# Kernel optimization log

Hardware: AMD Instinct MI355X
Metric: run time of the kernel (lower is better)

## Reference

```python
import jax, jax.numpy as jnp
import numpy as np

D_MODEL = 192
NODE_NUM = 64
DEPTH = 2
ALPHA = 0.05
NUM_LAYERS = 2
LN_EPS = 1e-5


def _gcn(x, p):
    # x: [N, in_dim*D_MODEL]; faithful port of GCN.forward (eval mode)
    nv1, nv2, ws, bs, wm, bm, we, be, wl, bl, g, b = p
    N = x.shape[0]
    in_dim = x.shape[1] // D_MODEL
    adp = jax.nn.softmax(jax.nn.relu(nv1 @ nv2), axis=1)            # [V,V]
    adj = adp + jnp.eye(NODE_NUM, dtype=x.dtype)
    a = adj / adj.sum(1, keepdims=True)                              # row-normalized
    h0 = jax.lax.conv_general_dilated(
        x.reshape(N, in_dim, D_MODEL), ws, (1,), 'VALID',
        dimension_numbers=('NCH', 'OIH', 'NCH')) + bs[None, :, None]  # [N,C,V]
    h = h0
    outs = [h0]
    for _ in range(DEPTH):
        h = ALPHA * h0 + (1.0 - ALPHA) * jnp.einsum('ncw,vw->ncv', h, a)
        outs.append(h)
    ho = jnp.concatenate(outs, axis=1)                               # [N,(DEPTH+1)C,V]
    ho = jax.nn.gelu(jnp.einsum('ncv,oc->nov', ho, wm) + bm[None, :, None], approximate=False)
    ho = jnp.einsum('ncv,oc->nov', ho, we) + be[None, :, None]       # [N,6,V]
    ho = jnp.einsum('nov,dv->nod', ho, wl) + bl                      # [N,6,D]
    mu = ho.mean(-1, keepdims=True)
    var = ((ho - mu) ** 2).mean(-1, keepdims=True)                   # biased, like torch LN
    ho = (ho - mu) / jnp.sqrt(var + LN_EPS) * g + b
    return ho.reshape(N, 6 * D_MODEL)


def _encoder(inp4, flag, layer_params):
    x = jnp.transpose(inp4, (2, 0, 1, 3)) if flag == 1 else jnp.transpose(inp4, (1, 0, 2, 3))
    W, B, O, D = x.shape
    L = W + O - 1
    N = W * B
    # input_transfer: shift row r by r along the slice axis
    place = jax.vmap(lambda xr, r: jax.lax.dynamic_update_slice(
        jnp.zeros((B, L, D), x.dtype), xr, (0, r, 0)))
    a = place(x, jnp.arange(W)).reshape(N, L, D)
    layer0_output = None
    output_all = None
    rows_layers, cols_layers = [], []
    for layer in range(NUM_LAYERS):
        if layer >= 1:
            a = output_all  # eval mode: F.dropout is identity
            if layer == 1:
                layer0_output = a
        p = layer_params[layer]

        def step(carry, x_t, p=p):
            h_row, h_col = carry
            gate = _gcn(jnp.concatenate([h_row, h_col, x_t], axis=-1), p)  # [N,6D]
            sg = jax.nn.sigmoid(gate[:, :4 * D])
            tg = jnp.tanh(gate[:, 4 * D:])
            ug_r, og_r, ug_c, og_c = jnp.split(sg, 4, axis=-1)
            ig_r, ig_c = jnp.split(tg, 2, axis=-1)
            h_row = jnp.tanh((1.0 - ug_r) * h_row + ug_r * ig_r) * og_r
            h_col = jnp.tanh((1.0 - ug_c) * h_col + ug_c * ig_c) * og_c
            out_s = jnp.concatenate([h_row, h_col], axis=-1)
            # col hidden is saved pre-roll, rolled for next step
            return (h_row, jnp.roll(h_col, B, axis=0)), (out_s, h_row, h_col)

        init = (jnp.zeros((N, D), x.dtype), jnp.zeros((N, D), x.dtype))
        _, (outs, hrows, hcols) = jax.lax.scan(step, init, jnp.swapaxes(a, 0, 1))
        output_all = jnp.swapaxes(outs, 0, 1)                        # [N,L,2D]
        if layer >= 1:
            output_all = output_all + layer0_output
        # rows saved at slice s>=O-1 from block loc = s-O+1
        rows = hrows.reshape(L, W, B, D)[jnp.arange(O - 1, L), jnp.arange(W)]  # [W,B,D]
        # cols saved at slice s>=W-1 from last batch block
        cols = hcols[W - 1:, (W - 1) * B:, :]                        # [O,B,D]
        rows_layers.append(rows)
        cols_layers.append(cols)
    hidden_row_all = jnp.stack(rows_layers).transpose(2, 0, 1, 3)    # [B,layers,W,D]
    hidden_col_all = jnp.stack(cols_layers).transpose(2, 0, 1, 3)    # [B,layers,O,D]
    if flag == 1:
        return output_all, hidden_col_all, hidden_row_all
    return output_all, hidden_row_all, hidden_col_all


def setup_inputs() -> dict:
    key = jax.random.key(0)
    ks = jax.random.split(key, 20)
    idx = [0]
    def nxt():
        k = ks[idx[0]]
        idx[0] += 1
        return k
    B, W, O = 8, 24, 48
    K = D_MODEL - NODE_NUM + 1  # 129
    cc, sc, nd = 16, 32, 40
    d = {"input": jax.random.normal(nxt(), (B, W, O, D_MODEL), dtype=jnp.float32)}
    for li, in_dim in enumerate([3, 4]):
        d[f"nodevec1_{li}"] = jax.random.normal(nxt(), (NODE_NUM, nd), dtype=jnp.float32)
        d[f"nodevec2_{li}"] = jax.random.normal(nxt(), (nd, NODE_NUM), dtype=jnp.float32)
        d[f"w_start_{li}"] = jax.random.normal(nxt(), (cc, in_dim, K), dtype=jnp.float32) * 0.05
        d[f"b_start_{li}"] = jnp.zeros((cc,), jnp.float32)
        d[f"w_mlp_{li}"] = jax.random.normal(nxt(), (sc, (DEPTH + 1) * cc), dtype=jnp.float32) * 0.05
        d[f"b_mlp_{li}"] = jnp.zeros((sc,), jnp.float32)
        d[f"w_end_{li}"] = jax.random.normal(nxt(), (6, sc), dtype=jnp.float32) * 0.05
        d[f"b_end_{li}"] = jnp.zeros((6,), jnp.float32)
        d[f"w_lin_{li}"] = jax.random.normal(nxt(), (D_MODEL, NODE_NUM), dtype=jnp.float32) * 0.05
        d[f"b_lin_{li}"] = jnp.zeros((D_MODEL,), jnp.float32)
        d[f"gamma_{li}"] = jnp.ones((D_MODEL,), jnp.float32)
        d[f"beta_{li}"] = jnp.zeros((D_MODEL,), jnp.float32)
    d["flag"] = 0
    return d


def reference(input, nodevec1_0, nodevec2_0, w_start_0, b_start_0, w_mlp_0, b_mlp_0,
              w_end_0, b_end_0, w_lin_0, b_lin_0, gamma_0, beta_0,
              nodevec1_1, nodevec2_1, w_start_1, b_start_1, w_mlp_1, b_mlp_1,
              w_end_1, b_end_1, w_lin_1, b_lin_1, gamma_1, beta_1, flag):
    p0 = (nodevec1_0, nodevec2_0, w_start_0, b_start_0, w_mlp_0, b_mlp_0,
          w_end_0, b_end_0, w_lin_0, b_lin_0, gamma_0, beta_0)
    p1 = (nodevec1_1, nodevec2_1, w_start_1, b_start_1, w_mlp_1, b_mlp_1,
          w_end_1, b_end_1, w_lin_1, b_lin_1, gamma_1, beta_1)
    return _encoder(input, flag, (p0, p1))
```

## Files before the change

kernel.cpp:

```cpp
#include <hip/hip_runtime.h>
#include <hip/hip_bf16.h>

#define NT 512
typedef unsigned short u16;

__device__ __forceinline__ u16 tobf(float x) {
  union { __hip_bfloat16 h; u16 u; } cv;
  cv.h = __float2bfloat16(x);
  return cv.u;
}
__device__ __forceinline__ float frombf(u16 u) {
  return __uint_as_float(((unsigned)u) << 16);
}
__device__ __forceinline__ float sigf(float x) {
  return __builtin_amdgcn_rcpf(1.f + __builtin_amdgcn_exp2f(-1.4426950408889634f * x));
}
__device__ __forceinline__ float tanh_fast(float x) {
  return 1.f - 2.f * __builtin_amdgcn_rcpf(1.f + __builtin_amdgcn_exp2f(2.8853900817779268f * x));
}

struct SeqArgs {
  const float* input;
  const float* nv1_0; const float* nv2_0; const float* nv1_1; const float* nv2_1;
  const float* w_start0; const float* b_start0; const float* w_mlp0; const float* b_mlp0;
  const float* w_end0;   const float* b_end0;   const float* w_lin0; const float* b_lin0;
  const float* gamma0;   const float* beta0;
  const float* w_start1; const float* b_start1; const float* w_mlp1; const float* b_mlp1;
  const float* w_end1;   const float* b_end1;   const float* w_lin1; const float* b_lin1;
  const float* gamma1;   const float* beta1;
  float* HCOL;
  int*   flags;
  float* out_all; float* out_hrow; float* out_hcol;
};

__global__ __launch_bounds__(NT, 2) void seq_kernel(SeqArgs A) {
  const int n = blockIdx.x, w = n >> 3, b = n & 7, tid = threadIdx.x;
  const int pred = (n + 184) % 192;

  __shared__ __align__(16) float sCIN[768];
  __shared__ __align__(16) u16   sWS[64 * 132];
  __shared__ __align__(16) float sAT[4096];
  __shared__ __align__(16) float sH[2][1024];
  __shared__ __align__(16) float sAbuf[4928];
  float* const sPart = sAbuf;
  float* const sG    = sAbuf;
  float* const sE    = sAbuf + 2048;
  float* const sY    = sAbuf;
  float* const smWE  = sAbuf + 3072;
  float* const smBE  = sAbuf + 3264;
  float* const smWM  = sAbuf + 3328;

  for (int layer = 0; layer < 2; ++layer) {
    const int in_dim = 3 + layer;
    const int P = in_dim - 1;
    const float* nv1    = layer ? A.nv1_1    : A.nv1_0;
    const float* nv2    = layer ? A.nv2_1    : A.nv2_0;
    const float* wstart = layer ? A.w_start1 : A.w_start0;
    const float* bs     = layer ? A.b_start1 : A.b_start0;
    const float* wm     = layer ? A.w_mlp1   : A.w_mlp0;
    const float* bm     = layer ? A.b_mlp1   : A.b_mlp0;
    const float* we     = layer ? A.w_end1   : A.w_end0;
    const float* be     = layer ? A.b_end1   : A.b_end0;
    const float* wl     = layer ? A.w_lin1   : A.w_lin0;
    const float* bl     = layer ? A.b_lin1   : A.b_lin0;
    const float* gm     = layer ? A.gamma1   : A.gamma0;
    const float* bt     = layer ? A.beta1    : A.beta0;

    for (int idx = tid; idx < 4096; idx += NT) {
      int v = idx >> 6, ww = idx & 63;
      float s = 0.f;
      for (int j = 0; j < 40; ++j) s = fmaf(nv1[v*40 + j], nv2[j*64 + ww], s);
      sAbuf[idx] = fmaxf(s, 0.f);
    }
    __syncthreads();
    if (tid < 64) {
      const int v = tid;
      float m = -1e30f;
      for (int ww = 0; ww < 64; ++ww) m = fmaxf(m, sAbuf[v*64 + ww]);
      float s = 0.f;
      for (int ww = 0; ww < 64; ++ww) { float e = expf(sAbuf[v*64 + ww] - m); sAbuf[v*64 + ww] = e; s += e; }
      float inv = 1.f / s, rs = 1.f;
      for (int ww = 0; ww < 64; ++ww) rs += sAbuf[v*64 + ww] * inv;
      float irs = 1.f / rs;
      for (int ww = 0; ww < 64; ++ww) {
        float a = sAbuf[v*64 + ww] * inv + ((ww == v) ? 1.f : 0.f);
        sAT[ww*64 + v] = a * irs;
      }
    }
    __syncthreads();
    for (int idx = tid; idx < 16*in_dim*132; idx += NT) {
      int row = idx / 132, k = idx - row*132;
      sWS[idx] = (k < 129) ? tobf(wstart[((row & 15)*in_dim + (row >> 4))*129 + k]) : (u16)0;
    }
    for (int idx = tid; idx < 1536; idx += NT) { int o = idx/48, c = idx - o*48; smWM[o*50 + c] = wm[idx]; }
    for (int idx = tid; idx < 192; idx += NT) smWE[idx] = we[idx];
    if (tid < 6) smBE[tid] = be[tid];
    for (int d = tid; d < 384; d += NT) sCIN[d] = 0.f;

    const int v_p = tid & 63;
    const int o0  = tid >> 6;
    const float bmv0 = bm[o0], bmv1 = bm[o0 + 8], bmv2 = bm[o0 + 16], bmv3 = bm[o0 + 24];
    float blv = 0.f, gmv = 1.f, btv = 0.f;
    if (tid < 384) blv = bl[(tid >= 192) ? tid - 192 : tid];
    if (tid < 192) { gmv = gm[tid]; btv = bt[tid]; }
    float bs_r[2];
    bs_r[0] = bs[tid >> 6];
    bs_r[1] = bs[(tid >> 6) + 8];
    __syncthreads();

    auto pre_phase = [&](int t) {
      if (layer == 0) {
        int o = t - w;
        if (o >= 0 && o < 48) {
          const float* xr = A.input + (((size_t)(b*24 + w)*48 + o)*192);
          for (int d = tid; d < 192; d += NT) sCIN[384 + d] = xr[d];
        } else {
          for (int d = tid; d < 192; d += NT) sCIN[384 + d] = 0.f;
        }
      } else {
        const float* xr = A.out_all + ((size_t)n*71 + t)*384;
        for (int d = tid; d < 384; d += NT) sCIN[384 + d] = xr[d];
      }
      __syncthreads();
      const int nslots = P << 8;
      for (int s = tid; s < nslots; s += NT) {
        const int cidx = s >> 4;
        const int p = cidx >> 4, c = cidx & 15;
        const int vg = s & 15;
        const int ich = (p == 0) ? 0 : (p + 1);
        const float* xin = ((p == 0) ? &sCIN[0] : &sCIN[384 + (p-1)*192]) + vg*4;
        const u16* wrow = &sWS[(ich*16 + c)*132];
        float a0 = 0.f, a1 = 0.f, a2 = 0.f, a3 = 0.f;
        float4 xc = *(const float4*)xin;
        for (int k4 = 0; k4 < 128; k4 += 4) {
          ushort4 wu = *(const ushort4*)(wrow + k4);
          float w0 = frombf(wu.x), w1 = frombf(wu.y), w2 = frombf(wu.z), w3 = frombf(wu.w);
          float4 xn = *(const float4*)(xin + k4 + 4);
          a0 = fmaf(w3, xc.w, fmaf(w2, xc.z, fmaf(w1, xc.y, fmaf(w0, xc.x, a0))));
          a1 = fmaf(w3, xn.x, fmaf(w2, xc.w, fmaf(w1, xc.z, fmaf(w0, xc.y, a1))));
          a2 = fmaf(w3, xn.y, fmaf(w2, xn.x, fmaf(w1, xc.w, fmaf(w0, xc.z, a2))));
          a3 = fmaf(w3, xn.z, fmaf(w2, xn.y, fmaf(w1, xn.x, fmaf(w0, xc.w, a3))));
          xc = xn;
        }
        float wk = frombf(wrow[128]);
        a0 = fmaf(wk, xc.x, a0); a1 = fmaf(wk, xc.y, a1);
        a2 = fmaf(wk, xc.z, a2); a3 = fmaf(wk, xc.w, a3);
        *(float4*)&sPart[cidx*64 + vg*4] = make_float4(a0, a1, a2, a3);
      }
      __syncthreads();
      {
        const int c0 = tid >> 6, v = tid & 63;
        float sum0 = bs_r[0], sum1 = bs_r[1];
        for (int p = 0; p < P; ++p) {
          sum0 += sPart[(p*16 + c0     )*64 + v];
          sum1 += sPart[(p*16 + c0 + 8 )*64 + v];
        }
        sH[0][ c0      *64 + v] = sum0;
        sH[0][(c0 + 8 )*64 + v] = sum1;
      }
      __syncthreads();
    };
    pre_phase(0);

    for (int t = 0; t < 71; ++t) {
      const int S = layer*71 + t;

      if (t > 0) {
        if (tid == 0) {
          while (__hip_atomic_load(&A.flags[pred*32], __ATOMIC_ACQUIRE, __HIP_MEMORY_SCOPE_AGENT) < S)
            __builtin_amdgcn_s_sleep(1);
        }
        __syncthreads();
        float* hc = A.HCOL + ((size_t)((S-1) & 31)*192 + pred)*192;
        for (int d = tid; d < 192; d += NT)
          sCIN[192 + d] = __hip_atomic_load(&hc[d], __ATOMIC_RELAXED, __HIP_MEMORY_SCOPE_AGENT);
        __syncthreads();
      }

      {
        const int c = tid >> 5, vg2 = tid & 31;
        const int vbase = c*64 + vg2*2;
        const float* xin = &sCIN[192 + vg2*2];
        const u16* wrow = &sWS[(16 + c)*132];
        float a0 = sH[0][vbase], a1 = sH[0][vbase + 1];
        float2 xc = *(const float2*)xin;
        for (int k2 = 0; k2 < 128; k2 += 2) {
          ushort2 wu = *(const ushort2*)(wrow + k2);
          float w0 = frombf(wu.x), w1 = frombf(wu.y);
          float2 xn = *(const float2*)(xin + k2 + 2);
          a0 = fmaf(w1, xc.y, fmaf(w0, xc.x, a0));
          a1 = fmaf(w1, xn.x, fmaf(w0, xc.y, a1));
          xc = xn;
        }
        float wk = frombf(wrow[128]);
        a0 = fmaf(wk, xc.x, a0); a1 = fmaf(wk, xc.y, a1);
        sH[0][vbase] = a0; sH[0][vbase + 1] = a1;
      }
      __syncthreads();

      float g0 = bmv0, g1 = bmv1, g2 = bmv2, g3 = bmv3;
      {
        const int c0 = o0 * 2;
        float pa0 = 0.f, pa1 = 0.f;
        for (int w4 = 0; w4 < 64; w4 += 4) {
          float a0v = sAT[(w4+0)*64 + v_p];
          float a1v = sAT[(w4+1)*64 + v_p];
          float a2v = sAT[(w4+2)*64 + v_p];
          float a3v = sAT[(w4+3)*64 + v_p];
          float4 h0v = *(const float4*)&sH[0][ c0      *64 + w4];
          float4 h1v = *(const float4*)&sH[0][(c0 + 1 )*64 + w4];
          pa0 = fmaf(h0v.x, a0v, pa0); pa0 = fmaf(h0v.y, a1v, pa0);
          pa0 = fmaf(h0v.z, a2v, pa0); pa0 = fmaf(h0v.w, a3v, pa0);
          pa1 = fmaf(h1v.x, a0v, pa1); pa1 = fmaf(h1v.y, a1v, pa1);
          pa1 = fmaf(h1v.z, a2v, pa1); pa1 = fmaf(h1v.w, a3v, pa1);
        }
        sH[1][ c0      *64 + v_p] = fmaf(0.95f, pa0, 0.05f * sH[0][ c0      *64 + v_p]);
        sH[1][(c0 + 1 )*64 + v_p] = fmaf(0.95f, pa1, 0.05f * sH[0][(c0 + 1 )*64 + v_p]);
        for (int c = 0; c < 16; ++c) {
          float hv = sH[0][c*64 + v_p];
          g0 = fmaf(smWM[(o0     )*50 + c], hv, g0);
          g1 = fmaf(smWM[(o0 +  8)*50 + c], hv, g1);
          g2 = fmaf(smWM[(o0 + 16)*50 + c], hv, g2);
          g3 = fmaf(smWM[(o0 + 24)*50 + c], hv, g3);
        }
      }
      __syncthreads();

      {
        const int c0 = o0 * 2;
        float pa0 = 0.f, pa1 = 0.f;
        for (int w4 = 0; w4 < 64; w4 += 4) {
          float a0v = sAT[(w4+0)*64 + v_p];
          float a1v = sAT[(w4+1)*64 + v_p];
          float a2v = sAT[(w4+2)*64 + v_p];
          float a3v = sAT[(w4+3)*64 + v_p];
          float4 h0v = *(const float4*)&sH[1][ c0      *64 + w4];
          float4 h1v = *(const float4*)&sH[1][(c0 + 1 )*64 + w4];
          pa0 = fmaf(h0v.x, a0v, pa0); pa0 = fmaf(h0v.y, a1v, pa0);
          pa0 = fmaf(h0v.z, a2v, pa0); pa0 = fmaf(h0v.w, a3v, pa0);
          pa1 = fmaf(h1v.x, a0v, pa1); pa1 = fmaf(h1v.y, a1v, pa1);
          pa1 = fmaf(h1v.z, a2v, pa1); pa1 = fmaf(h1v.w, a3v, pa1);
        }
        float h00 = sH[0][ c0      *64 + v_p];
        float h01 = sH[0][(c0 + 1 )*64 + v_p];
        sH[0][ c0      *64 + v_p] = fmaf(0.95f, pa0, 0.05f * h00);
        sH[0][(c0 + 1 )*64 + v_p] = fmaf(0.95f, pa1, 0.05f * h01);
        for (int c = 0; c < 16; ++c) {
          float hv = sH[1][c*64 + v_p];
          g0 = fmaf(smWM[(o0     )*50 + 16 + c], hv, g0);
          g1 = fmaf(smWM[(o0 +  8)*50 + 16 + c], hv, g1);
          g2 = fmaf(smWM[(o0 + 16)*50 + 16 + c], hv, g2);
          g3 = fmaf(smWM[(o0 + 24)*50 + 16 + c], hv, g3);
        }
      }
      __syncthreads();

      {
        for (int c = 0; c < 16; ++c) {
          float hv = sH[0][c*64 + v_p];
          g0 = fmaf(smWM[(o0     )*50 + 32 + c], hv, g0);
          g1 = fmaf(smWM[(o0 +  8)*50 + 32 + c], hv, g1);
          g2 = fmaf(smWM[(o0 + 16)*50 + 32 + c], hv, g2);
          g3 = fmaf(smWM[(o0 + 24)*50 + 32 + c], hv, g3);
        }
        g0 = 0.5f * g0 * (1.f + erff(g0 * 0.70710678118654752f));
        g1 = 0.5f * g1 * (1.f + erff(g1 * 0.70710678118654752f));
        g2 = 0.5f * g2 * (1.f + erff(g2 * 0.70710678118654752f));
        g3 = 0.5f * g3 * (1.f + erff(g3 * 0.70710678118654752f));
        sG[(o0     )*64 + v_p] = g0;
        sG[(o0 +  8)*64 + v_p] = g1;
        sG[(o0 + 16)*64 + v_p] = g2;
        sG[(o0 + 24)*64 + v_p] = g3;
      }
      __syncthreads();

      for (int idx = tid; idx < 384; idx += NT) {
        int o2 = idx >> 6, v = idx & 63;
        float acc = smBE[o2];
        for (int c = 0; c < 32; ++c) acc = fmaf(smWE[o2*32 + c], sG[c*64 + v], acc);
        sE[idx] = acc;
      }
      __syncthreads();

      if (tid < 384) {
        const int d  = (tid >= 192) ? tid - 192 : tid;
        const int r0 = (tid >= 192) ? 3 : 0;
        const float4* wrow = (const float4*)(wl + d*64);
        float y0 = blv, y1 = blv, y2 = blv;
        for (int q = 0; q < 16; ++q) {
          float4 wv = wrow[q];
          float4 e0 = *(const float4*)&sE[(r0+0)*64 + q*4];
          float4 e1 = *(const float4*)&sE[(r0+1)*64 + q*4];
          float4 e2 = *(const float4*)&sE[(r0+2)*64 + q*4];
          y0 = fmaf(e0.x,wv.x, fmaf(e0.y,wv.y, fmaf(e0.z,wv.z, fmaf(e0.w,wv.w, y0))));
          y1 = fmaf(e1.x,wv.x, fmaf(e1.y,wv.y, fmaf(e1.z,wv.z, fmaf(e1.w,wv.w, y1))));
          y2 = fmaf(e2.x,wv.x, fmaf(e2.y,wv.y, fmaf(e2.z,wv.z, fmaf(e2.w,wv.w, y2))));
        }
        sY[(r0+0)*192 + d] = y0;
        sY[(r0+1)*192 + d] = y1;
        sY[(r0+2)*192 + d] = y2;
      }
      __syncthreads();

      if (tid < 192) {
        const int r = tid >> 5, l32 = tid & 31;
        float sm = 0.f, sq = 0.f;
#pragma unroll
        for (int m = 0; m < 6; ++m) {
          float v = sY[r*192 + l32 + 32*m];
          sm += v; sq = fmaf(v, v, sq);
        }
#pragma unroll
        for (int off = 16; off >= 1; off >>= 1) {
          sm += __shfl_xor(sm, off);
          sq += __shfl_xor(sq, off);
        }
        if (l32 == 0) {
          float mu = sm * (1.f/192.f);
          float var = sq * (1.f/192.f) - mu*mu;
          sH[1][r] = mu;
          sH[1][8 + r] = rsqrtf(fmaxf(var, 0.f) + 1e-5f);
        }
      }
      __syncthreads();

      float hcn = 0.f;
      if (tid < 192) {
        const int d = tid;
        float y2 = fmaf((sY[2*192+d] - sH[1][2]) * sH[1][10], gmv, btv);
        float y3 = fmaf((sY[3*192+d] - sH[1][3]) * sH[1][11], gmv, btv);
        float y5 = fmaf((sY[5*192+d] - sH[1][5]) * sH[1][13], gmv, btv);
        float ugc = sigf(y2), ogc = sigf(y3), igc = tanh_fast(y5);
        float hc = sCIN[192 + d];
        hcn = tanh_fast(fmaf(ugc, igc, (1.f - ugc)*hc)) * ogc;
        __hip_atomic_store(&A.HCOL[((size_t)(S & 31)*192 + n)*192 + d], hcn,
                           __ATOMIC_RELAXED, __HIP_MEMORY_SCOPE_AGENT);
      }
      __syncthreads();
      if (tid == 0) {
        __threadfence();
        __hip_atomic_store(&A.flags[n*32], S + 1, __ATOMIC_RELEASE, __HIP_MEMORY_SCOPE_AGENT);
      }
      if (tid < 192) {
        const int d = tid;
        float y0 = fmaf((sY[0*192+d] - sH[1][0]) * sH[1][8],  gmv, btv);
        float y1 = fmaf((sY[1*192+d] - sH[1][1]) * sH[1][9],  gmv, btv);
        float y4 = fmaf((sY[4*192+d] - sH[1][4]) * sH[1][12], gmv, btv);
        float ugr = sigf(y0), ogr = sigf(y1), igr = tanh_fast(y4);
        float hr = sCIN[d];
        float hrn = tanh_fast(fmaf(ugr, igr, (1.f - ugr)*hr)) * ogr;
        sCIN[d] = hrn;
        float* oa = A.out_all + ((size_t)n*71 + t)*384;
        if (layer == 0) { oa[d] = hrn; oa[192 + d] = hcn; }
        else           { oa[d] = hrn + sCIN[384 + d]; oa[192 + d] = hcn + sCIN[576 + d]; }
        if (t == 47 + w)
          A.out_hrow[(((size_t)b*2 + layer)*24 + w)*192 + d] = hrn;
        if (w == 23 && t >= 23)
          A.out_hcol[(((size_t)b*2 + layer)*48 + (t - 23))*192 + d] = hcn;
      }
      __syncthreads();
      if (t < 70) pre_phase(t + 1);
    }
    __syncthreads();
  }
}

extern "C" void kernel_launch(void* const* d_in, const int* in_sizes, int n_in,
                              void* d_out, int out_size, void* d_ws, size_t ws_size,
                              hipStream_t stream) {
  (void)in_sizes; (void)n_in; (void)out_size; (void)ws_size;
  char* ws = (char*)d_ws;
  int*   flags = (int*)ws;
  float* HCOL  = (float*)(ws + 24576);

  hipMemsetAsync(flags, 0, 24576, stream);

  SeqArgs A;
  A.input    = (const float*)d_in[0];
  A.nv1_0    = (const float*)d_in[1];  A.nv2_0 = (const float*)d_in[2];
  A.w_start0 = (const float*)d_in[3];  A.b_start0 = (const float*)d_in[4];
  A.w_mlp0   = (const float*)d_in[5];  A.b_mlp0   = (const float*)d_in[6];
  A.w_end0   = (const float*)d_in[7];  A.b_end0   = (const float*)d_in[8];
  A.w_lin0   = (const float*)d_in[9];  A.b_lin0   = (const float*)d_in[10];
  A.gamma0   = (const float*)d_in[11]; A.beta0    = (const float*)d_in[12];
  A.nv1_1    = (const float*)d_in[13]; A.nv2_1 = (const float*)d_in[14];
  A.w_start1 = (const float*)d_in[15]; A.b_start1 = (const float*)d_in[16];
  A.w_mlp1   = (const float*)d_in[17]; A.b_mlp1   = (const float*)d_in[18];
  A.w_end1   = (const float*)d_in[19]; A.b_end1   = (const float*)d_in[20];
  A.w_lin1   = (const float*)d_in[21]; A.b_lin1   = (const float*)d_in[22];
  A.gamma1   = (const float*)d_in[23]; A.beta1    = (const float*)d_in[24];
  A.HCOL = HCOL; A.flags = flags;
  A.out_all  = (float*)d_out;
  A.out_hrow = (float*)d_out + 5234688;
  A.out_hcol = (float*)d_out + 5308416;

  seq_kernel<<<192, NT, 0, stream>>>(A);
}
```

Before: 2.739 ms.

## Replace block barriers with wave-local LDS fences and relax cross-block flag handshake

The two propagation steps now run back-to-back inside each wave, separated only by an LDS waitcnt fence instead of __syncthreads. This relies on each wave reading only the sH rows it wrote itself. The three mlp channel accumulations are merged into one unrolled loop after a single barrier, with the second hop stored in a separate scratch area. The inter-block handshake now has 192 threads poll the flag with relaxed loads and read HCOL directly, and the producer swaps __threadfence plus a release store for a vmcnt wait plus a relaxed store. Together these cut barrier and fence latency on the serial step chain, at the cost of weaker memory-ordering guarantees across CUs.

```diff
diff --git a/kernel.cpp b/kernel.cpp
--- a/kernel.cpp
+++ b/kernel.cpp
@@ -17,6 +17,10 @@
 }
 __device__ __forceinline__ float tanh_fast(float x) {
   return 1.f - 2.f * __builtin_amdgcn_rcpf(1.f + __builtin_amdgcn_exp2f(2.8853900817779268f * x));
+}
+__device__ __forceinline__ void lds_fence() {
+  asm volatile("s_waitcnt lgkmcnt(0)" ::: "memory");
+  __builtin_amdgcn_sched_barrier(0);
 }
 
 struct SeqArgs {
@@ -44,6 +48,7 @@
   __shared__ __align__(16) float sAbuf[4928];
   float* const sPart = sAbuf;
   float* const sG    = sAbuf;
+  float* const sH2c  = sAbuf + 2048;
   float* const sE    = sAbuf + 2048;
   float* const sY    = sAbuf;
   float* const smWE  = sAbuf + 3072;
@@ -166,14 +171,14 @@
       const int S = layer*71 + t;
 
       if (t > 0) {
-        if (tid == 0) {
-          while (__hip_atomic_load(&A.flags[pred*32], __ATOMIC_ACQUIRE, __HIP_MEMORY_SCOPE_AGENT) < S)
+        if (tid < 192) {
+          while (__hip_atomic_load(&A.flags[pred*32], __ATOMIC_RELAXED, __HIP_MEMORY_SCOPE_AGENT) < S)
             __builtin_amdgcn_s_sleep(1);
-        }
-        __syncthreads();
-        float* hc = A.HCOL + ((size_t)((S-1) & 31)*192 + pred)*192;
-        for (int d = tid; d < 192; d += NT)
-          sCIN[192 + d] = __hip_atomic_load(&hc[d], __ATOMIC_RELAXED, __HIP_MEMORY_SCOPE_AGENT);
+          __builtin_amdgcn_sched_barrier(0);
+          asm volatile("" ::: "memory");
+          const float* hc = A.HCOL + ((size_t)((S-1) & 31)*192 + pred)*192;
+          sCIN[192 + tid] = __hip_atomic_load(&hc[tid], __ATOMIC_RELAXED, __HIP_MEMORY_SCOPE_AGENT);
+        }
         __syncthreads();
       }
 
@@ -196,9 +201,7 @@
         a0 = fmaf(wk, xc.x, a0); a1 = fmaf(wk, xc.y, a1);
         sH[0][vbase] = a0; sH[0][vbase + 1] = a1;
       }
-      __syncthreads();
-
-      float g0 = bmv0, g1 = bmv1, g2 = bmv2, g3 = bmv3;
+      lds_fence();
       {
         const int c0 = o0 * 2;
         float pa0 = 0.f, pa1 = 0.f;
@@ -214,21 +217,12 @@
           pa1 = fmaf(h1v.x, a0v, pa1); pa1 = fmaf(h1v.y, a1v, pa1);
           pa1 = fmaf(h1v.z, a2v, pa1); pa1 = fmaf(h1v.w, a3v, pa1);
         }
-        sH[1][ c0      *64 + v_p] = fmaf(0.95f, pa0, 0.05f * sH[0][ c0      *64 + v_p]);
-        sH[1][(c0 + 1 )*64 + v_p] = fmaf(0.95f, pa1, 0.05f * sH[0][(c0 + 1 )*64 + v_p]);
-        for (int c = 0; c < 16; ++c) {
-          float hv = sH[0][c*64 + v_p];
-          g0 = fmaf(smWM[(o0     )*50 + c], hv, g0);
-          g1 = fmaf(smWM[(o0 +  8)*50 + c], hv, g1);
-          g2 = fmaf(smWM[(o0 + 16)*50 + c], hv, g2);
-          g3 = fmaf(smWM[(o0 + 24)*50 + c], hv, g3);
-        }
-      }
-      __syncthreads();
-
-      {
-        const int c0 = o0 * 2;
-        float pa0 = 0.f, pa1 = 0.f;
+        float h0a = sH[0][ c0      *64 + v_p];
+        float h0b = sH[0][(c0 + 1 )*64 + v_p];
+        sH[1][ c0      *64 + v_p] = fmaf(0.95f, pa0, 0.05f * h0a);
+        sH[1][(c0 + 1 )*64 + v_p] = fmaf(0.95f, pa1, 0.05f * h0b);
+        lds_fence();
+        float pb0 = 0.f, pb1 = 0.f;
         for (int w4 = 0; w4 < 64; w4 += 4) {
           float a0v = sAT[(w4+0)*64 + v_p];
           float a1v = sAT[(w4+1)*64 + v_p];
@@ -236,32 +230,27 @@
           float a3v = sAT[(w4+3)*64 + v_p];
           float4 h0v = *(const float4*)&sH[1][ c0      *64 + w4];
           float4 h1v = *(const float4*)&sH[1][(c0 + 1 )*64 + w4];
-          pa0 = fmaf(h0v.x, a0v, pa0); pa0 = fmaf(h0v.y, a1v, pa0);
-          pa0 = fmaf(h0v.z, a2v, pa0); pa0 = fmaf(h0v.w, a3v, pa0);
-          pa1 = fmaf(h1v.x, a0v, pa1); pa1 = fmaf(h1v.y, a1v, pa1);
-          pa1 = fmaf(h1v.z, a2v, pa1); pa1 = fmaf(h1v.w, a3v, pa1);
-        }
-        float h00 = sH[0][ c0      *64 + v_p];
-        float h01 = sH[0][(c0 + 1 )*64 + v_p];
-        sH[0][ c0      *64 + v_p] = fmaf(0.95f, pa0, 0.05f * h00);
-        sH[0][(c0 + 1 )*64 + v_p] = fmaf(0.95f, pa1, 0.05f * h01);
+          pb0 = fmaf(h0v.x, a0v, pb0); pb0 = fmaf(h0v.y, a1v, pb0);
+          pb0 = fmaf(h0v.z, a2v, pb0); pb0 = fmaf(h0v.w, a3v, pb0);
+          pb1 = fmaf(h1v.x, a0v, pb1); pb1 = fmaf(h1v.y, a1v, pb1);
+          pb1 = fmaf(h1v.z, a2v, pb1); pb1 = fmaf(h1v.w, a3v, pb1);
+        }
+        sH2c[ c0      *64 + v_p] = fmaf(0.95f, pb0, 0.05f * h0a);
+        sH2c[(c0 + 1 )*64 + v_p] = fmaf(0.95f, pb1, 0.05f * h0b);
+      }
+      __syncthreads();
+
+      {
+        float g0 = bmv0, g1 = bmv1, g2 = bmv2, g3 = bmv3;
+#pragma unroll
         for (int c = 0; c < 16; ++c) {
-          float hv = sH[1][c*64 + v_p];
-          g0 = fmaf(smWM[(o0     )*50 + 16 + c], hv, g0);
-          g1 = fmaf(smWM[(o0 +  8)*50 + 16 + c], hv, g1);
-          g2 = fmaf(smWM[(o0 + 16)*50 + 16 + c], hv, g2);
-          g3 = fmaf(smWM[(o0 + 24)*50 + 16 + c], hv, g3);
-        }
-      }
-      __syncthreads();
-
-      {
-        for (int c = 0; c < 16; ++c) {
-          float hv = sH[0][c*64 + v_p];
-          g0 = fmaf(smWM[(o0     )*50 + 32 + c], hv, g0);
-          g1 = fmaf(smWM[(o0 +  8)*50 + 32 + c], hv, g1);
-          g2 = fmaf(smWM[(o0 + 16)*50 + 32 + c], hv, g2);
-          g3 = fmaf(smWM[(o0 + 24)*50 + 32 + c], hv, g3);
+          float h0v = sH[0][c*64 + v_p];
+          float h1v = sH[1][c*64 + v_p];
+          float h2v = sH2c[c*64 + v_p];
+          g0 = fmaf(smWM[(o0     )*50 + c], h0v, fmaf(smWM[(o0     )*50 + 16 + c], h1v, fmaf(smWM[(o0     )*50 + 32 + c], h2v, g0)));
+          g1 = fmaf(smWM[(o0 +  8)*50 + c], h0v, fmaf(smWM[(o0 +  8)*50 + 16 + c], h1v, fmaf(smWM[(o0 +  8)*50 + 32 + c], h2v, g1)));
+          g2 = fmaf(smWM[(o0 + 16)*50 + c], h0v, fmaf(smWM[(o0 + 16)*50 + 16 + c], h1v, fmaf(smWM[(o0 + 16)*50 + 32 + c], h2v, g2)));
+          g3 = fmaf(smWM[(o0 + 24)*50 + c], h0v, fmaf(smWM[(o0 + 24)*50 + 16 + c], h1v, fmaf(smWM[(o0 + 24)*50 + 32 + c], h2v, g3)));
         }
         g0 = 0.5f * g0 * (1.f + erff(g0 * 0.70710678118654752f));
         g1 = 0.5f * g1 * (1.f + erff(g1 * 0.70710678118654752f));
@@ -338,8 +327,8 @@
       }
       __syncthreads();
       if (tid == 0) {
-        __threadfence();
-        __hip_atomic_store(&A.flags[n*32], S + 1, __ATOMIC_RELEASE, __HIP_MEMORY_SCOPE_AGENT);
+        asm volatile("s_waitcnt vmcnt(0)" ::: "memory");
+        __hip_atomic_store(&A.flags[n*32], S + 1, __ATOMIC_RELAXED, __HIP_MEMORY_SCOPE_AGENT);
       }
       if (tid < 192) {
         const int d = tid;
```

After: 2.707 ms. About the same (-1.1%).
